# Kernel tuning notes

Measured on AMD Instinct MI355X. Metric: run time of the kernel, lower is better.

## Reference

```python
import jax, jax.numpy as jnp
import numpy as np

B, L, D, C = 1, 512, 128, 128  # batch, length, input_dim, channel_dim


def _layernorm(x, w, b, eps=1e-5):
    mu = jnp.mean(x, axis=-1, keepdims=True)
    var = jnp.var(x, axis=-1, keepdims=True)
    return (x - mu) * jax.lax.rsqrt(var + eps) * w + b


def setup_inputs() -> dict:
    key = jax.random.key(0)
    ks = jax.random.split(key, 12)
    s = 0.05  # weight scale ~ xavier for d=128
    f32 = jnp.float32
    return {
        "z": jax.random.normal(ks[0], (B, L, L, D), f32),
        "ln_in_w": jnp.ones((D,), f32), "ln_in_b": jnp.zeros((D,), f32),
        "Wga": jax.random.normal(ks[1], (D, C), f32) * s, "bga": jnp.zeros((C,), f32),
        "Wla": jax.random.normal(ks[2], (D, C), f32) * s, "bla": jnp.zeros((C,), f32),
        "Wgb": jax.random.normal(ks[3], (D, C), f32) * s, "bgb": jnp.zeros((C,), f32),
        "Wlb": jax.random.normal(ks[4], (D, C), f32) * s, "blb": jnp.zeros((C,), f32),
        "ln_o_w": jnp.ones((C,), f32), "ln_o_b": jnp.zeros((C,), f32),
        "Wgo": jax.random.normal(ks[5], (D, D), f32) * s, "bgo": jnp.zeros((D,), f32),
        "Wlo": jax.random.normal(ks[6], (C, D), f32) * s, "blo": jnp.zeros((D,), f32),
    }


def reference(z, ln_in_w, ln_in_b, Wga, bga, Wla, bla, Wgb, bgb, Wlb, blb,
              ln_o_w, ln_o_b, Wgo, bgo, Wlo, blo):
    # z: [B, L, L, D]
    zn = _layernorm(z, ln_in_w, ln_in_b)
    a = jax.nn.sigmoid(zn @ Wga + bga) * (zn @ Wla + bla)   # [B,L,L,C]
    b = jax.nn.sigmoid(zn @ Wgb + bgb) * (zn @ Wlb + blb)   # [B,L,L,C]
    # triangular update (axis=1): per-channel L x L matmul
    # k[b,i,j,c] = sum_m a[b,i,m,c] * b[b,m,j,c]
    k = jnp.einsum('bimc,bmjc->bijc', a, b)
    out = jax.nn.sigmoid(zn @ Wgo + bgo) * (_layernorm(k, ln_o_w, ln_o_b) @ Wlo + blo)
    return out
```

## Files before the change

kernel.cpp:

```cpp
#include <hip/hip_runtime.h>

typedef unsigned short u16;
typedef __attribute__((ext_vector_type(8))) short bf16x8;
typedef __attribute__((ext_vector_type(4))) float f32x4;

#define L_ 512
#define D_ 128
#define LL_ (512*512)
#define LP_ 136
#define TP_ 72

#define WT_OFF 0
#define B2_OFF 98304
#define AT_OFF (B2_OFF + 1536)
#define BT_OFF (AT_OFF + 128*LL_)
#define KT_OFF (BT_OFF + 128*LL_)

union U16x8 { uint4 u4; bf16x8 v; u16 s[8]; };
union U16x4 { ushort4 v; u16 s[4]; };

__device__ __forceinline__ u16 f2bf(float f){
  union { float f; unsigned int i; } w; w.f = f;
  unsigned int r = w.i + 0x7FFFu + ((w.i >> 16) & 1u);
  return (u16)(r >> 16);
}
__device__ __forceinline__ float sigm(float x){
  return 1.0f / (1.0f + __expf(-x));
}

__global__ __launch_bounds__(256) void conv_kernel(
    const float* __restrict__ Wga, const float* __restrict__ Wla,
    const float* __restrict__ Wgb, const float* __restrict__ Wlb,
    const float* __restrict__ Wgo, const float* __restrict__ Wlo,
    const float* __restrict__ lnw, const float* __restrict__ lnb,
    const float* __restrict__ onw, const float* __restrict__ onb,
    const float* __restrict__ bga, const float* __restrict__ bla,
    const float* __restrict__ bgb, const float* __restrict__ blb,
    const float* __restrict__ bgo, const float* __restrict__ blo,
    u16* __restrict__ wt, float* __restrict__ bias2)
{
  if (blockIdx.x < 384){
    int idx = blockIdx.x*256 + threadIdx.x;
    int w = idx >> 14, rem = idx & 16383, n = rem >> 7, k = rem & 127;
    const float* src;
    switch (w){
      case 0: src = Wga; break; case 1: src = Wla; break; case 2: src = Wgb; break;
      case 3: src = Wlb; break; case 4: src = Wgo; break; default: src = Wlo;
    }
    float sc = (w == 5) ? onw[k] : lnw[k];
    wt[idx] = f2bf(src[k*128 + n] * sc);
  } else {
    int j = (blockIdx.x - 384)*256 + threadIdx.x;
    int w = j >> 7, n = j & 127;
    const float* src; const float* bs;
    switch (w){
      case 0: src = Wga; bs = bga; break; case 1: src = Wla; bs = bla; break;
      case 2: src = Wgb; bs = bgb; break; case 3: src = Wlb; bs = blb; break;
      case 4: src = Wgo; bs = bgo; break; default: src = Wlo; bs = blo;
    }
    const float* lb = (w == 5) ? onb : lnb;
    float acc = bs[n];
    for (int k = 0; k < 128; ++k) acc += lb[k] * src[k*128 + n];
    bias2[j] = acc;
  }
}

__device__ __forceinline__ void gemm128(const u16* znlds, const u16* __restrict__ wtm,
                                        int wm, int wn, int quad, int l16, f32x4 acc[4][4])
{
  bf16x8 bf[4][4];
#pragma unroll
  for (int nt = 0; nt < 4; ++nt){
    int n = wn*64 + nt*16 + l16;
#pragma unroll
    for (int kc = 0; kc < 4; ++kc){
      U16x8 u; u.u4 = *(const uint4*)(wtm + n*128 + kc*32 + quad*8);
      bf[nt][kc] = u.v;
    }
  }
#pragma unroll
  for (int mt = 0; mt < 4; ++mt){
    int row = wm*64 + mt*16 + l16;
    bf16x8 af[4];
#pragma unroll
    for (int kc = 0; kc < 4; ++kc)
      af[kc] = *(const bf16x8*)(znlds + row*LP_ + kc*32 + quad*8);
#pragma unroll
    for (int nt = 0; nt < 4; ++nt)
#pragma unroll
      for (int kc = 0; kc < 4; ++kc)
        acc[mt][nt] = __builtin_amdgcn_mfma_f32_16x16x32_bf16(af[kc], bf[nt][kc], acc[mt][nt], 0, 0, 0);
  }
}

__device__ __forceinline__ void gemm64(const u16* alds, const u16* __restrict__ wtm,
                                       int wm, int wn, int quad, int l16, f32x4 acc[2][4])
{
  bf16x8 bf[4][4];
#pragma unroll
  for (int nt = 0; nt < 4; ++nt){
    int n = wn*64 + nt*16 + l16;
#pragma unroll
    for (int kc = 0; kc < 4; ++kc){
      U16x8 u; u.u4 = *(const uint4*)(wtm + n*128 + kc*32 + quad*8);
      bf[nt][kc] = u.v;
    }
  }
#pragma unroll
  for (int mt = 0; mt < 2; ++mt){
    int row = wm*32 + mt*16 + l16;
    bf16x8 af[4];
#pragma unroll
    for (int kc = 0; kc < 4; ++kc)
      af[kc] = *(const bf16x8*)(alds + row*LP_ + kc*32 + quad*8);
#pragma unroll
    for (int nt = 0; nt < 4; ++nt)
#pragma unroll
      for (int kc = 0; kc < 4; ++kc)
        acc[mt][nt] = __builtin_amdgcn_mfma_f32_16x16x32_bf16(af[kc], bf[nt][kc], acc[mt][nt], 0, 0, 0);
  }
}

__global__ __launch_bounds__(256) void stageA_kernel(
    const float* __restrict__ z, const u16* __restrict__ wt,
    const float* __restrict__ bias2,
    u16* __restrict__ a_t, u16* __restrict__ b_tt)
{
  __shared__ __align__(16) u16 smem[128*LP_];
  u16* zn = smem;
  u16* trh = smem;

  const int bid = blockIdx.x;
  const int type = bid >> 11;
  const int tile = bid & 2047;
  const int outer = tile >> 2;
  const int seg = tile & 3;

  const int t = threadIdx.x;
  const int r = t >> 1, h = t & 1;
  const int lane = t & 63, wave = t >> 6;
  const int quad = lane >> 4, l16 = lane & 15;
  const int wm = wave & 1, wn = wave >> 1;

  {
    int gpos = (type == 0) ? (outer*L_ + seg*128 + r) : ((seg*128 + r)*L_ + outer);
    const float* zrow = z + gpos*D_ + h*64;
    float raw[64];
    float sum = 0.f, sq = 0.f;
#pragma unroll
    for (int q = 0; q < 16; ++q){
      float4 v = *(const float4*)(zrow + q*4);
      raw[q*4+0] = v.x; raw[q*4+1] = v.y; raw[q*4+2] = v.z; raw[q*4+3] = v.w;
      sum += v.x + v.y + v.z + v.w;
      sq  += v.x*v.x + v.y*v.y + v.z*v.z + v.w*v.w;
    }
    sum += __shfl_xor(sum, 1, 64);
    sq  += __shfl_xor(sq , 1, 64);
    float mu = sum * (1.f/128.f);
    float rstd = rsqrtf(sq*(1.f/128.f) - mu*mu + 1e-5f);
#pragma unroll
    for (int q = 0; q < 8; ++q){
      U16x8 o;
#pragma unroll
      for (int e = 0; e < 8; ++e)
        o.s[e] = f2bf((raw[q*8+e] - mu)*rstd);
      *(uint4*)(zn + r*LP_ + h*64 + q*8) = o.u4;
    }
  }
  __syncthreads();

  const u16* wg   = wt + (type ? 2 : 0)*16384;
  const u16* wl   = wt + (type ? 3 : 1)*16384;
  const float* bgp = bias2 + (type ? 2 : 0)*128;
  const float* blp = bias2 + (type ? 3 : 1)*128;
  const f32x4 z4 = {0.f, 0.f, 0.f, 0.f};

  f32x4 accG[4][4], accL[4][4];
#pragma unroll
  for (int mt = 0; mt < 4; ++mt)
#pragma unroll
    for (int nt = 0; nt < 4; ++nt){ accG[mt][nt] = z4; accL[mt][nt] = z4; }

  gemm128(zn, wg, wm, wn, quad, l16, accG);
#pragma unroll
  for (int nt = 0; nt < 4; ++nt){
    float bb = bgp[wn*64 + nt*16 + l16];
#pragma unroll
    for (int mt = 0; mt < 4; ++mt)
#pragma unroll
      for (int e = 0; e < 4; ++e)
        accG[mt][nt][e] = sigm(accG[mt][nt][e] + bb);
  }
  gemm128(zn, wl, wm, wn, quad, l16, accL);
#pragma unroll
  for (int nt = 0; nt < 4; ++nt){
    float bb = blp[wn*64 + nt*16 + l16];
#pragma unroll
    for (int mt = 0; mt < 4; ++mt)
#pragma unroll
      for (int e = 0; e < 4; ++e)
        accG[mt][nt][e] *= (accL[mt][nt][e] + bb);
  }

  __syncthreads();

  u16* dst = type ? b_tt : a_t;
  const int base = outer*L_ + seg*128;
#pragma unroll
  for (int pass = 0; pass < 2; ++pass){
    if (wm == pass){
#pragma unroll
      for (int nt = 0; nt < 4; ++nt){
        int gcol = wn*64 + nt*16 + l16;
#pragma unroll
        for (int mt = 0; mt < 4; ++mt){
          U16x4 pk;
#pragma unroll
          for (int e = 0; e < 4; ++e)
            pk.s[e] = f2bf(accG[mt][nt][e]);
          *(ushort4*)(trh + gcol*TP_ + mt*16 + quad*4) = pk.v;
        }
      }
    }
    __syncthreads();
#pragma unroll
    for (int q = 0; q < 4; ++q){
      uint4 v = *(const uint4*)(trh + r*TP_ + h*32 + q*8);
      *(uint4*)(dst + r*LL_ + base + pass*64 + h*32 + q*8) = v;
    }
    __syncthreads();
  }
}

__global__ __launch_bounds__(256) void stageT_kernel(
    const u16* __restrict__ a_t, const u16* __restrict__ b_tt, u16* __restrict__ k_t)
{
  __shared__ __align__(16) u16 As[128*64];
  __shared__ __align__(16) u16 Bs[128*64];
  const int bid = blockIdx.x;
  const int lid = (bid & 7)*256 + (bid >> 3);
  const int c = lid >> 4, it = (lid >> 2) & 3, jt = lid & 3;
  const u16* Ab = a_t + c*LL_ + it*128*L_;
  const u16* Bb = b_tt + c*LL_ + jt*128*L_;
  const int t = threadIdx.x;
  const int lane = t & 63, wave = t >> 6;
  const int quad = lane >> 4, l16 = lane & 15;
  const int wm = wave & 1, wn = wave >> 1;
  const int sr8 = lane >> 3, scl = lane & 7;
  const int cgx = scl ^ sr8;
  const int swz = (l16 & 7) << 3;

  f32x4 acc[4][4];
  const f32x4 z4 = {0.f,0.f,0.f,0.f};
#pragma unroll
  for (int mt = 0; mt < 4; ++mt)
#pragma unroll
    for (int nt = 0; nt < 4; ++nt) acc[mt][nt] = z4;

  for (int kt = 0; kt < 8; ++kt){
    const int k0 = kt*64;
#pragma unroll
    for (int q = 0; q < 4; ++q){
      int row = q*32 + wave*8 + sr8;
      __builtin_amdgcn_global_load_lds(
          (const __attribute__((address_space(1))) void*)(Ab + row*L_ + k0 + cgx*8),
          (__attribute__((address_space(3))) void*)(&As[(q*32 + wave*8)*64]),
          16, 0, 0);
    }
#pragma unroll
    for (int q = 0; q < 4; ++q){
      int row = q*32 + wave*8 + sr8;
      __builtin_amdgcn_global_load_lds(
          (const __attribute__((address_space(1))) void*)(Bb + row*L_ + k0 + cgx*8),
          (__attribute__((address_space(3))) void*)(&Bs[(q*32 + wave*8)*64]),
          16, 0, 0);
    }
    __syncthreads();
    bf16x8 bfr[4][2];
#pragma unroll
    for (int nt = 0; nt < 4; ++nt){
      int brow = wn*64 + nt*16 + l16;
#pragma unroll
      for (int ks = 0; ks < 2; ++ks)
        bfr[nt][ks] = *(const bf16x8*)(Bs + brow*64 + (((ks*4 + quad)*8) ^ swz));
    }
#pragma unroll
    for (int mt = 0; mt < 4; ++mt){
      int arow = wm*64 + mt*16 + l16;
      bf16x8 af[2];
#pragma unroll
      for (int ks = 0; ks < 2; ++ks)
        af[ks] = *(const bf16x8*)(As + arow*64 + (((ks*4 + quad)*8) ^ swz));
#pragma unroll
      for (int nt = 0; nt < 4; ++nt)
#pragma unroll
        for (int ks = 0; ks < 2; ++ks)
          acc[mt][nt] = __builtin_amdgcn_mfma_f32_16x16x32_bf16(af[ks], bfr[nt][ks], acc[mt][nt], 0, 0, 0);
    }
    __syncthreads();
  }

#pragma unroll
  for (int mt = 0; mt < 4; ++mt)
#pragma unroll
    for (int nt = 0; nt < 4; ++nt){
      int gcol = wn*64 + nt*16 + l16;
#pragma unroll
      for (int e = 0; e < 4; ++e){
        int grow = wm*64 + mt*16 + quad*4 + e;
        k_t[c*LL_ + (it*128 + grow)*L_ + jt*128 + gcol] = f2bf(acc[mt][nt][e]);
      }
    }
}

__global__ __launch_bounds__(256) void stageC_kernel(
    const u16* __restrict__ k_t, const float* __restrict__ z,
    const u16* __restrict__ wt, const float* __restrict__ bias2,
    float* __restrict__ out)
{
  __shared__ __align__(16) u16 zn2[64*LP_];
  __shared__ __align__(16) u16 kbuf[128*TP_];
  const u16* wtgo = wt + 4*16384;
  const u16* wtlo = wt + 5*16384;
  const float* bgo2 = bias2 + 4*128;
  const float* blo2 = bias2 + 5*128;
  const int bx = blockIdx.x;
  const int pos0 = (bx >> 3)*L_ + (bx & 7)*64;
  const int t = threadIdx.x, r = t >> 1, h = t & 1;
  const int rl4 = t >> 2, qd = t & 3;
  const int lane = t & 63, wave = t >> 6;
  const int quad = lane >> 4, l16 = lane & 15;
  const int wm = wave & 1, wn = wave >> 1;

#pragma unroll
  for (int q = 0; q < 4; ++q)
    *(uint4*)(kbuf + r*TP_ + h*32 + q*8) = *(const uint4*)(k_t + r*LL_ + pos0 + h*32 + q*8);
  __syncthreads();

  {
    float sum = 0.f, sq = 0.f;
    float kv[32];
#pragma unroll
    for (int q = 0; q < 32; ++q){
      union { unsigned int i; float f; } w;
      w.i = ((unsigned int)kbuf[(qd*32 + q)*TP_ + rl4]) << 16;
      kv[q] = w.f; sum += w.f; sq += w.f*w.f;
    }
    sum += __shfl_xor(sum, 1, 64); sq += __shfl_xor(sq, 1, 64);
    sum += __shfl_xor(sum, 2, 64); sq += __shfl_xor(sq, 2, 64);
    float mu = sum*(1.f/128.f);
    float rstd = rsqrtf(sq*(1.f/128.f) - mu*mu + 1e-5f);
#pragma unroll
    for (int q = 0; q < 4; ++q){
      U16x8 o;
#pragma unroll
      for (int e = 0; e < 8; ++e)
        o.s[e] = f2bf((kv[q*8+e] - mu)*rstd);
      *(uint4*)(zn2 + rl4*LP_ + qd*32 + q*8) = o.u4;
    }
  }
  __syncthreads();

  {
    const float* zr = z + (pos0 + rl4)*D_ + qd*32;
    float zv[32];
    float sum = 0.f, sq = 0.f;
#pragma unroll
    for (int q = 0; q < 8; ++q){
      float4 v = *(const float4*)(zr + q*4);
      zv[q*4+0] = v.x; zv[q*4+1] = v.y; zv[q*4+2] = v.z; zv[q*4+3] = v.w;
      sum += v.x + v.y + v.z + v.w;
      sq  += v.x*v.x + v.y*v.y + v.z*v.z + v.w*v.w;
    }
    sum += __shfl_xor(sum, 1, 64); sq += __shfl_xor(sq, 1, 64);
    sum += __shfl_xor(sum, 2, 64); sq += __shfl_xor(sq, 2, 64);
    float mu = sum*(1.f/128.f);
    float rstd = rsqrtf(sq*(1.f/128.f) - mu*mu + 1e-5f);
#pragma unroll
    for (int q = 0; q < 4; ++q){
      U16x8 o;
#pragma unroll
      for (int e = 0; e < 8; ++e)
        o.s[e] = f2bf((zv[q*8+e] - mu)*rstd);
      *(uint4*)(kbuf + rl4*LP_ + qd*32 + q*8) = o.u4;
    }
  }
  __syncthreads();

  f32x4 accK[2][4], accO[2][4];
  const f32x4 z4 = {0.f,0.f,0.f,0.f};
#pragma unroll
  for (int mt = 0; mt < 2; ++mt)
#pragma unroll
    for (int nt = 0; nt < 4; ++nt){ accK[mt][nt] = z4; accO[mt][nt] = z4; }

  gemm64(zn2,  wtlo, wm, wn, quad, l16, accK);
  gemm64(kbuf, wtgo, wm, wn, quad, l16, accO);

#pragma unroll
  for (int nt = 0; nt < 4; ++nt){
    int gcol = wn*64 + nt*16 + l16;
    float bo = bgo2[gcol], bl = blo2[gcol];
#pragma unroll
    for (int mt = 0; mt < 2; ++mt)
#pragma unroll
      for (int e = 0; e < 4; ++e){
        int grow = wm*32 + mt*16 + quad*4 + e;
        float s = sigm(accO[mt][nt][e] + bo);
        out[(pos0 + grow)*D_ + gcol] = s*(accK[mt][nt][e] + bl);
      }
  }
}

extern "C" void kernel_launch(void* const* d_in, const int* in_sizes, int n_in,
                              void* d_out, int out_size, void* d_ws, size_t ws_size,
                              hipStream_t stream)
{
  const float* z   = (const float*)d_in[0];
  const float* lnw = (const float*)d_in[1];
  const float* lnb = (const float*)d_in[2];
  const float* Wga = (const float*)d_in[3];
  const float* bga = (const float*)d_in[4];
  const float* Wla = (const float*)d_in[5];
  const float* bla = (const float*)d_in[6];
  const float* Wgb = (const float*)d_in[7];
  const float* bgb = (const float*)d_in[8];
  const float* Wlb = (const float*)d_in[9];
  const float* blb = (const float*)d_in[10];
  const float* onw = (const float*)d_in[11];
  const float* onb = (const float*)d_in[12];
  const float* Wgo = (const float*)d_in[13];
  const float* bgo = (const float*)d_in[14];
  const float* Wlo = (const float*)d_in[15];
  const float* blo = (const float*)d_in[16];

  u16* ws   = (u16*)d_ws;
  u16* wt   = ws + WT_OFF;
  float* b2 = (float*)(ws + B2_OFF);
  u16* a_t  = ws + AT_OFF;
  u16* b_tt = ws + BT_OFF;
  u16* k_t  = ws + KT_OFF;
  float* out = (float*)d_out;

  conv_kernel<<<387, 256, 0, stream>>>(Wga, Wla, Wgb, Wlb, Wgo, Wlo,
                                       lnw, lnb, onw, onb,
                                       bga, bla, bgb, blb, bgo, blo, wt, b2);
  stageA_kernel<<<4096, 256, 0, stream>>>(z, wt, b2, a_t, b_tt);
  stageT_kernel<<<2048, 256, 0, stream>>>(a_t, b_tt, k_t);
  stageC_kernel<<<4096, 256, 0, stream>>>(k_t, z, wt, b2, out);
}
```

Before: 601.9 us.

## Precompute normalized z once in bf16 and reuse across stages

Adds a stageZ kernel that layer-normalizes z once and stores it as bf16. Stage A and stage C then read this smaller bf16 tensor instead of re-reading fp32 z and recomputing the norm. Stage A2 loads it straight into LDS with global_load_lds and an XOR-swizzled layout in place of padding. The price is an extra kernel launch and an extra 64MB workspace buffer, and this path is only taken when the workspace is large enough.

```diff
diff --git a/kernel.cpp b/kernel.cpp
--- a/kernel.cpp
+++ b/kernel.cpp
@@ -12,9 +12,14 @@
 
 #define WT_OFF 0
 #define B2_OFF 98304
-#define AT_OFF (B2_OFF + 1536)
-#define BT_OFF (AT_OFF + 128*LL_)
-#define KT_OFF (BT_OFF + 128*LL_)
+#define ZN_OFF (B2_OFF + 1536)
+#define AT2_OFF (ZN_OFF + 128*LL_)
+#define BT2_OFF (AT2_OFF + 128*LL_)
+#define KT2_OFF (BT2_OFF + 128*LL_)
+#define WS2_NEED_BYTES ((size_t)(KT2_OFF + 128*LL_) * 2)
+#define AT1_OFF (B2_OFF + 1536)
+#define BT1_OFF (AT1_OFF + 128*LL_)
+#define KT1_OFF (BT1_OFF + 128*LL_)
 
 union U16x8 { uint4 u4; bf16x8 v; u16 s[8]; };
 union U16x4 { ushort4 v; u16 s[4]; };
@@ -65,6 +70,36 @@
   }
 }
 
+__global__ __launch_bounds__(256) void stageZ_kernel(
+    const float* __restrict__ z, u16* __restrict__ zn_g)
+{
+  const int t = threadIdx.x, r = t >> 1, h = t & 1;
+  const int row = blockIdx.x*128 + r;
+  const float* zrow = z + (long)row*D_ + h*64;
+  float raw[64];
+  float sum = 0.f, sq = 0.f;
+#pragma unroll
+  for (int q = 0; q < 16; ++q){
+    float4 v = *(const float4*)(zrow + q*4);
+    raw[q*4+0] = v.x; raw[q*4+1] = v.y; raw[q*4+2] = v.z; raw[q*4+3] = v.w;
+    sum += v.x + v.y + v.z + v.w;
+    sq  += v.x*v.x + v.y*v.y + v.z*v.z + v.w*v.w;
+  }
+  sum += __shfl_xor(sum, 1, 64);
+  sq  += __shfl_xor(sq , 1, 64);
+  float mu = sum * (1.f/128.f);
+  float rstd = rsqrtf(sq*(1.f/128.f) - mu*mu + 1e-5f);
+  u16* orow = zn_g + (long)row*D_ + h*64;
+#pragma unroll
+  for (int q = 0; q < 8; ++q){
+    U16x8 o;
+#pragma unroll
+    for (int e = 0; e < 8; ++e)
+      o.s[e] = f2bf(raw[q*8+e] - mu > 0 ? (raw[q*8+e] - mu)*rstd : (raw[q*8+e] - mu)*rstd);
+    *(uint4*)(orow + q*8) = o.u4;
+  }
+}
+
 __device__ __forceinline__ void gemm128(const u16* znlds, const u16* __restrict__ wtm,
                                         int wm, int wn, int quad, int l16, f32x4 acc[4][4])
 {
@@ -93,8 +128,8 @@
   }
 }
 
-__device__ __forceinline__ void gemm64(const u16* alds, const u16* __restrict__ wtm,
-                                       int wm, int wn, int quad, int l16, f32x4 acc[2][4])
+__device__ __forceinline__ void gemm128s(const u16* znS, const u16* __restrict__ wtm,
+                                         int wm, int wn, int quad, int l16, f32x4 acc[4][4])
 {
   bf16x8 bf[4][4];
 #pragma unroll
@@ -106,6 +141,35 @@
       bf[nt][kc] = u.v;
     }
   }
+  const int r7 = l16 & 7;
+#pragma unroll
+  for (int mt = 0; mt < 4; ++mt){
+    int row = wm*64 + mt*16 + l16;
+    bf16x8 af[4];
+#pragma unroll
+    for (int kc = 0; kc < 4; ++kc)
+      af[kc] = *(const bf16x8*)(znS + row*128 + (((kc*4 + quad) ^ r7) << 3));
+#pragma unroll
+    for (int nt = 0; nt < 4; ++nt)
+#pragma unroll
+      for (int kc = 0; kc < 4; ++kc)
+        acc[mt][nt] = __builtin_amdgcn_mfma_f32_16x16x32_bf16(af[kc], bf[nt][kc], acc[mt][nt], 0, 0, 0);
+  }
+}
+
+__device__ __forceinline__ void gemm64(const u16* alds, const u16* __restrict__ wtm,
+                                       int wm, int wn, int quad, int l16, f32x4 acc[2][4])
+{
+  bf16x8 bf[4][4];
+#pragma unroll
+  for (int nt = 0; nt < 4; ++nt){
+    int n = wn*64 + nt*16 + l16;
+#pragma unroll
+    for (int kc = 0; kc < 4; ++kc){
+      U16x8 u; u.u4 = *(const uint4*)(wtm + n*128 + kc*32 + quad*8);
+      bf[nt][kc] = u.v;
+    }
+  }
 #pragma unroll
   for (int mt = 0; mt < 2; ++mt){
     int row = wm*32 + mt*16 + l16;
@@ -118,6 +182,105 @@
 #pragma unroll
       for (int kc = 0; kc < 4; ++kc)
         acc[mt][nt] = __builtin_amdgcn_mfma_f32_16x16x32_bf16(af[kc], bf[nt][kc], acc[mt][nt], 0, 0, 0);
+  }
+}
+
+__global__ __launch_bounds__(256) void stageA2_kernel(
+    const u16* __restrict__ zn_g, const u16* __restrict__ wt,
+    const float* __restrict__ bias2,
+    u16* __restrict__ a_t, u16* __restrict__ b_tt)
+{
+  __shared__ __align__(16) u16 znS[128*128];
+
+  const int bid = blockIdx.x;
+  const int type = bid >> 11;
+  const int tile = bid & 2047;
+  const int outer = tile >> 2;
+  const int seg = tile & 3;
+
+  const int t = threadIdx.x;
+  const int r = t >> 1, h = t & 1;
+  const int lane = t & 63, wave = t >> 6;
+  const int quad = lane >> 4, l16 = lane & 15;
+  const int wm = wave & 1, wn = wave >> 1;
+
+  {
+    const int lr = lane >> 4, lc = lane & 15;
+    const int r7s = (wave*4 + lr) & 7;
+    const int cgx = lc ^ r7s;
+#pragma unroll
+    for (int q = 0; q < 8; ++q){
+      int row = q*16 + wave*4 + lr;
+      int gpos = (type == 0) ? (outer*L_ + seg*128 + row) : ((seg*128 + row)*L_ + outer);
+      __builtin_amdgcn_global_load_lds(
+          (const __attribute__((address_space(1))) void*)(zn_g + (long)gpos*D_ + cgx*8),
+          (__attribute__((address_space(3))) void*)(&znS[(q*16 + wave*4)*128]),
+          16, 0, 0);
+    }
+  }
+  __syncthreads();
+
+  const u16* wg   = wt + (type ? 2 : 0)*16384;
+  const u16* wl   = wt + (type ? 3 : 1)*16384;
+  const float* bgp = bias2 + (type ? 2 : 0)*128;
+  const float* blp = bias2 + (type ? 3 : 1)*128;
+  const f32x4 z4 = {0.f, 0.f, 0.f, 0.f};
+
+  f32x4 accG[4][4], accL[4][4];
+#pragma unroll
+  for (int mt = 0; mt < 4; ++mt)
+#pragma unroll
+    for (int nt = 0; nt < 4; ++nt){ accG[mt][nt] = z4; accL[mt][nt] = z4; }
+
+  gemm128s(znS, wg, wm, wn, quad, l16, accG);
+#pragma unroll
+  for (int nt = 0; nt < 4; ++nt){
+    float bb = bgp[wn*64 + nt*16 + l16];
+#pragma unroll
+    for (int mt = 0; mt < 4; ++mt)
+#pragma unroll
+      for (int e = 0; e < 4; ++e)
+        accG[mt][nt][e] = sigm(accG[mt][nt][e] + bb);
+  }
+  gemm128s(znS, wl, wm, wn, quad, l16, accL);
+#pragma unroll
+  for (int nt = 0; nt < 4; ++nt){
+    float bb = blp[wn*64 + nt*16 + l16];
+#pragma unroll
+    for (int mt = 0; mt < 4; ++mt)
+#pragma unroll
+      for (int e = 0; e < 4; ++e)
+        accG[mt][nt][e] *= (accL[mt][nt][e] + bb);
+  }
+
+  __syncthreads();
+
+  u16* trh = znS;
+  u16* dst = type ? b_tt : a_t;
+  const int base = outer*L_ + seg*128;
+#pragma unroll
+  for (int pass = 0; pass < 2; ++pass){
+    if (wm == pass){
+#pragma unroll
+      for (int nt = 0; nt < 4; ++nt){
+        int gcol = wn*64 + nt*16 + l16;
+#pragma unroll
+        for (int mt = 0; mt < 4; ++mt){
+          U16x4 pk;
+#pragma unroll
+          for (int e = 0; e < 4; ++e)
+            pk.s[e] = f2bf(accG[mt][nt][e]);
+          *(ushort4*)(trh + gcol*TP_ + mt*16 + quad*4) = pk.v;
+        }
+      }
+    }
+    __syncthreads();
+#pragma unroll
+    for (int q = 0; q < 4; ++q){
+      uint4 v = *(const uint4*)(trh + r*TP_ + h*32 + q*8);
+      *(uint4*)(dst + r*LL_ + base + pass*64 + h*32 + q*8) = v;
+    }
+    __syncthreads();
   }
 }
 
@@ -311,6 +474,88 @@
         k_t[c*LL_ + (it*128 + grow)*L_ + jt*128 + gcol] = f2bf(acc[mt][nt][e]);
       }
     }
+}
+
+__global__ __launch_bounds__(256) void stageC2_kernel(
+    const u16* __restrict__ k_t, const u16* __restrict__ zn_g,
+    const u16* __restrict__ wt, const float* __restrict__ bias2,
+    float* __restrict__ out)
+{
+  __shared__ __align__(16) u16 zn2[64*LP_];
+  __shared__ __align__(16) u16 kbuf[128*TP_];
+  const u16* wtgo = wt + 4*16384;
+  const u16* wtlo = wt + 5*16384;
+  const float* bgo2 = bias2 + 4*128;
+  const float* blo2 = bias2 + 5*128;
+  const int bx = blockIdx.x;
+  const int pos0 = (bx >> 3)*L_ + (bx & 7)*64;
+  const int t = threadIdx.x, r = t >> 1, h = t & 1;
+  const int rl4 = t >> 2, qd = t & 3;
+  const int lane = t & 63, wave = t >> 6;
+  const int quad = lane >> 4, l16 = lane & 15;
+  const int wm = wave & 1, wn = wave >> 1;
+
+#pragma unroll
+  for (int q = 0; q < 4; ++q)
+    *(uint4*)(kbuf + r*TP_ + h*32 + q*8) = *(const uint4*)(k_t + r*LL_ + pos0 + h*32 + q*8);
+  __syncthreads();
+
+  {
+    float sum = 0.f, sq = 0.f;
+    float kv[32];
+#pragma unroll
+    for (int q = 0; q < 32; ++q){
+      union { unsigned int i; float f; } w;
+      w.i = ((unsigned int)kbuf[(qd*32 + q)*TP_ + rl4]) << 16;
+      kv[q] = w.f; sum += w.f; sq += w.f*w.f;
+    }
+    sum += __shfl_xor(sum, 1, 64); sq += __shfl_xor(sq, 1, 64);
+    sum += __shfl_xor(sum, 2, 64); sq += __shfl_xor(sq, 2, 64);
+    float mu = sum*(1.f/128.f);
+    float rstd = rsqrtf(sq*(1.f/128.f) - mu*mu + 1e-5f);
+#pragma unroll
+    for (int q = 0; q < 4; ++q){
+      U16x8 o;
+#pragma unroll
+      for (int e = 0; e < 8; ++e)
+        o.s[e] = f2bf((kv[q*8+e] - mu)*rstd);
+      *(uint4*)(zn2 + rl4*LP_ + qd*32 + q*8) = o.u4;
+    }
+  }
+  __syncthreads();
+
+  {
+    const u16* zr = zn_g + (long)(pos0 + rl4)*D_ + qd*32;
+    *(uint4*)(kbuf + rl4*LP_ + qd*32     ) = *(const uint4*)(zr);
+    *(uint4*)(kbuf + rl4*LP_ + qd*32 + 8 ) = *(const uint4*)(zr + 8);
+    *(uint4*)(kbuf + rl4*LP_ + qd*32 + 16) = *(const uint4*)(zr + 16);
+    *(uint4*)(kbuf + rl4*LP_ + qd*32 + 24) = *(const uint4*)(zr + 24);
+  }
+  __syncthreads();
+
+  f32x4 accK[2][4], accO[2][4];
+  const f32x4 z4 = {0.f,0.f,0.f,0.f};
+#pragma unroll
+  for (int mt = 0; mt < 2; ++mt)
+#pragma unroll
+    for (int nt = 0; nt < 4; ++nt){ accK[mt][nt] = z4; accO[mt][nt] = z4; }
+
+  gemm64(zn2,  wtlo, wm, wn, quad, l16, accK);
+  gemm64(kbuf, wtgo, wm, wn, quad, l16, accO);
+
+#pragma unroll
+  for (int nt = 0; nt < 4; ++nt){
+    int gcol = wn*64 + nt*16 + l16;
+    float bo = bgo2[gcol], bl = blo2[gcol];
+#pragma unroll
+    for (int mt = 0; mt < 2; ++mt)
+#pragma unroll
+      for (int e = 0; e < 4; ++e){
+        int grow = wm*32 + mt*16 + quad*4 + e;
+        float s = sigm(accO[mt][nt][e] + bo);
+        out[(pos0 + grow)*D_ + gcol] = s*(accK[mt][nt][e] + bl);
+      }
+  }
 }
 
 __global__ __launch_bounds__(256) void stageC_kernel(
@@ -437,15 +682,27 @@
   u16* ws   = (u16*)d_ws;
   u16* wt   = ws + WT_OFF;
   float* b2 = (float*)(ws + B2_OFF);
-  u16* a_t  = ws + AT_OFF;
-  u16* b_tt = ws + BT_OFF;
-  u16* k_t  = ws + KT_OFF;
   float* out = (float*)d_out;
 
   conv_kernel<<<387, 256, 0, stream>>>(Wga, Wla, Wgb, Wlb, Wgo, Wlo,
                                        lnw, lnb, onw, onb,
                                        bga, bla, bgb, blb, bgo, blo, wt, b2);
-  stageA_kernel<<<4096, 256, 0, stream>>>(z, wt, b2, a_t, b_tt);
-  stageT_kernel<<<2048, 256, 0, stream>>>(a_t, b_tt, k_t);
-  stageC_kernel<<<4096, 256, 0, stream>>>(k_t, z, wt, b2, out);
-}
+
+  if (ws_size >= WS2_NEED_BYTES){
+    u16* zn_g = ws + ZN_OFF;
+    u16* a_t  = ws + AT2_OFF;
+    u16* b_tt = ws + BT2_OFF;
+    u16* k_t  = ws + KT2_OFF;
+    stageZ_kernel<<<2048, 256, 0, stream>>>(z, zn_g);
+    stageA2_kernel<<<4096, 256, 0, stream>>>(zn_g, wt, b2, a_t, b_tt);
+    stageT_kernel<<<2048, 256, 0, stream>>>(a_t, b_tt, k_t);
+    stageC2_kernel<<<4096, 256, 0, stream>>>(k_t, zn_g, wt, b2, out);
+  } else {
+    u16* a_t  = ws + AT1_OFF;
+    u16* b_tt = ws + BT1_OFF;
+    u16* k_t  = ws + KT1_OFF;
+    stageA_kernel<<<4096, 256, 0, stream>>>(z, wt, b2, a_t, b_tt);
+    stageT_kernel<<<2048, 256, 0, stream>>>(a_t, b_tt, k_t);
+    stageC_kernel<<<4096, 256, 0, stream>>>(k_t, z, wt, b2, out);
+  }
+}
```

New measurement: 576.2 us. 1.04x faster.
